# Kernel optimization log

Hardware: AMD Instinct MI355X
Metric: run time of the kernel (lower is better)

Reference implementation:

```python
import jax, jax.numpy as jnp
import numpy as np

B, N, S, K = 8, 2048, 1024, 64     # clouds, points/cloud, fps samples (ratio=0.5), max neighbors
R2 = 0.2 ** 2                      # radius^2
C_IN, H1, C_OUT = 64, 128, 256     # PointNetConv nn = MLP([67, 128, 256])


def _fps(pos):
    """Farthest point sampling on one cloud. pos: [N,3] -> [S] int32 indices (deterministic start at point 0)."""
    dist = jnp.sum((pos - pos[0]) ** 2, axis=-1)
    idxs = jnp.zeros((S,), jnp.int32)
    def body(i, carry):
        idxs, dist = carry
        nxt = jnp.argmax(dist).astype(jnp.int32)
        dist = jnp.minimum(dist, jnp.sum((pos - pos[nxt]) ** 2, axis=-1))
        return (idxs.at[i].set(nxt), dist)
    idxs, _ = jax.lax.fori_loop(1, S, body, (idxs, dist))
    return idxs


def setup_inputs() -> dict:
    key = jax.random.key(0)
    k = jax.random.split(key, 4)
    x = jax.random.normal(k[0], (B * N, C_IN), dtype=jnp.float32)
    pos = jax.random.uniform(k[1], (B * N, 3), dtype=jnp.float32)
    batch = jnp.repeat(jnp.arange(B, dtype=jnp.int32), N)
    w1 = jax.random.normal(k[2], (C_IN + 3, H1), dtype=jnp.float32) / np.sqrt(C_IN + 3).astype(np.float32)
    b1 = jnp.zeros((H1,), jnp.float32)
    w2 = jax.random.normal(k[3], (H1, C_OUT), dtype=jnp.float32) / np.sqrt(H1).astype(np.float32)
    b2 = jnp.zeros((C_OUT,), jnp.float32)
    return {"x": x, "pos": pos, "batch": batch, "w1": w1, "b1": b1, "w2": w2, "b2": b2}


def reference(x, pos, batch, w1, b1, w2, b2):
    xb = x.reshape(B, N, C_IN)
    posb = pos.reshape(B, N, 3)
    idx = jax.vmap(_fps)(posb)                                            # [B,S] fps centers
    q = jnp.take_along_axis(posb, idx[:, :, None], axis=1)                # [B,S,3] sampled positions
    # radius ball query: up to K nearest points within R of each center
    d2 = jnp.sum((q[:, :, None, :] - posb[:, None, :, :]) ** 2, axis=-1)  # [B,S,N]
    vals, nbr = jax.lax.top_k(jnp.where(d2 <= R2, -d2, -jnp.inf), K)      # [B,S,K]
    valid = jnp.isfinite(vals)                                            # padded slots -> False
    # gather edge features (PointNetConv message: nn(cat([x_j, pos_j - pos_i])))
    x_j = jax.vmap(lambda xc, nc: xc[nc])(xb, nbr)                        # [B,S,K,C_IN]
    pos_j = jax.vmap(lambda pc, nc: pc[nc])(posb, nbr)                    # [B,S,K,3]
    feat = jnp.concatenate([x_j, pos_j - q[:, :, None, :]], axis=-1)      # [B,S,K,C_IN+3]
    h = jax.nn.relu(feat @ w1 + b1) @ w2 + b2                             # [B,S,K,C_OUT]
    # masked max-aggregation over the neighborhood (empty -> 0, matching PyG scatter-max default)
    h = jnp.where(valid[..., None], h, -jnp.inf)
    out = jnp.max(h, axis=2)
    out = jnp.where(jnp.isfinite(out), out, 0.0)                          # [B,S,C_OUT]
    batch_out = jnp.repeat(jnp.arange(B, dtype=batch.dtype), S)
    return out.reshape(B * S, C_OUT), q.reshape(B * S, 3), batch_out
```

## Files before the change

kernel.cpp:

```cpp
#include <hip/hip_runtime.h>
#include <math.h>

#define BQ 8
#define NQ 2048
#define SQ 1024
#define KQ 64
#define CIN 64
#define H1Q 128
#define COUT 256
#define R2F 0.04f
#define CAP 512
#define XW_ROWS 16
#define XW_BLOCKS ((BQ*NQ)/XW_ROWS)
#define W2C_BLOCKS 16

typedef float f32x2 __attribute__((ext_vector_type(2)));
typedef float f32x4v __attribute__((ext_vector_type(4)));
typedef short bf16x8 __attribute__((ext_vector_type(8)));
typedef unsigned int u32;
typedef unsigned short u16;

__device__ __forceinline__ u16 f2bf(float f) {
    u32 u = __builtin_bit_cast(u32, f);
    return (u16)((u + 0x7FFFu + ((u >> 16) & 1u)) >> 16);
}

template <int CTRL>
__device__ __forceinline__ float maxdpp(float x) {
    int xi = __builtin_bit_cast(int, x);
    int yi = __builtin_amdgcn_update_dpp((int)0xFF800000, xi, CTRL, 0xF, 0xF, false);
    return fmaxf(x, __builtin_bit_cast(float, yi));
}

__global__ __launch_bounds__(256)
void fps_xw_kernel(const float* __restrict__ pos, int* __restrict__ idx_out,
                   float* __restrict__ q_out, float* __restrict__ batch_out,
                   const float* __restrict__ x, const float* __restrict__ w1,
                   const float* __restrict__ b1, float* __restrict__ xw,
                   const float* __restrict__ w2, u16* __restrict__ w2f) {
#pragma clang fp contract(off)
    __shared__ float lnpos[NQ][4];
    __shared__ int   sel[SQ];
    __shared__ alignas(16) u32 red[2][8];

    const int tid = threadIdx.x;

    if (blockIdx.x >= 8 + XW_BLOCKS) {
        const int cb   = (blockIdx.x - (8 + XW_BLOCKS)) * 4 + (tid >> 6);
        const int lane = tid & 63;
        const int w  = cb >> 4, ct = (cb >> 2) & 3, kt = cb & 3;
        const int n  = w*64 + ct*16 + (lane & 15);
        const int k0 = kt*32 + (lane >> 4)*8;
        u32 pk[4];
#pragma unroll
        for (int jp = 0; jp < 4; ++jp) {
            u16 lo = f2bf(w2[(size_t)(k0 + 2*jp    )*COUT + n]);
            u16 hi = f2bf(w2[(size_t)(k0 + 2*jp + 1)*COUT + n]);
            pk[jp] = (u32)lo | ((u32)hi << 16);
        }
        u32* dst = (u32*)(w2f + ((size_t)cb*64 + lane)*8);
        dst[0] = pk[0]; dst[1] = pk[1]; dst[2] = pk[2]; dst[3] = pk[3];
        return;
    }

    if (blockIdx.x >= 8) {
        __shared__ float xs[XW_ROWS][CIN];
        const int r0 = (blockIdx.x - 8) * XW_ROWS;
        for (int i = tid; i < XW_ROWS*CIN; i += 256)
            xs[i >> 6][i & 63] = x[(size_t)(r0 + (i >> 6))*CIN + (i & 63)];
        __syncthreads();
        const int h = tid & 127, rbase = (tid >> 7) * 8;
        float acc[8];
        float bb = b1[h];
#pragma unroll
        for (int r = 0; r < 8; ++r) acc[r] = bb;
        for (int c = 0; c < CIN; ++c) {
            float wv = w1[c*H1Q + h];
#pragma unroll
            for (int r = 0; r < 8; ++r)
                acc[r] = fmaf(xs[rbase + r][c], wv, acc[r]);
        }
#pragma unroll
        for (int r = 0; r < 8; ++r)
            xw[(size_t)(r0 + rbase + r)*H1Q + h] = acc[r];
        return;
    }

    const int b = blockIdx.x;
    const int lane = tid & 63, wid = tid >> 6;
    const float* p = pos + (size_t)b * NQ * 3;

    f32x2 px[4], py[4], pz[4], dist[4];
#pragma unroll
    for (int r = 0; r < 4; ++r) {
        int i0 = tid * 8 + 2 * r;
        float x0 = p[3*i0],   y0 = p[3*i0+1], z0 = p[3*i0+2];
        float x1 = p[3*i0+3], y1 = p[3*i0+4], z1 = p[3*i0+5];
        px[r] = (f32x2){x0, x1}; py[r] = (f32x2){y0, y1}; pz[r] = (f32x2){z0, z1};
        lnpos[i0][0]   = -x0; lnpos[i0][1]   = -y0; lnpos[i0][2]   = -z0; lnpos[i0][3]   = 0.f;
        lnpos[i0+1][0] = -x1; lnpos[i0+1][1] = -y1; lnpos[i0+1][2] = -z1; lnpos[i0+1][3] = 0.f;
    }
    if (tid == 0) sel[0] = 0;
    __syncthreads();

    float cx = p[0], cy = p[1], cz = p[2];
    float lmax;
    {
        f32x2 ncx = (f32x2){-cx, -cx}, ncy = (f32x2){-cy, -cy}, ncz = (f32x2){-cz, -cz};
        lmax = -INFINITY;
#pragma unroll
        for (int r = 0; r < 4; ++r) {
            f32x2 dx = px[r] + ncx, dy = py[r] + ncy, dz = pz[r] + ncz;
            f32x2 a = dx * dx, bb = dy * dy, cc = dz * dz;
            f32x2 s = (a + bb) + cc;
            dist[r] = s;
            lmax = fmaxf(fmaxf(lmax, s.x), s.y);
        }
    }

    for (int s = 1; s < SQ; ++s) {
        const int par = s & 1;

        int ra = 1000, rb = 1000;
#pragma unroll
        for (int r = 3; r >= 0; --r) {
            ra = (dist[r].x == lmax) ? 2*r     : ra;
            rb = (dist[r].y == lmax) ? 2*r + 1 : rb;
        }
        int ridx = min(ra, rb);

        float m = lmax;
        m = maxdpp<0x111>(m);
        m = maxdpp<0x112>(m);
        m = maxdpp<0x114>(m);
        m = maxdpp<0x118>(m);
        m = maxdpp<0x142>(m);
        m = maxdpp<0x143>(m);
        float wmax = __builtin_bit_cast(
            float, __builtin_amdgcn_readlane(__builtin_bit_cast(int, m), 63));

        unsigned long long msk = __ballot(lmax == wmax);
        int wl = __ffsll(msk) - 1;
        int rw = __builtin_amdgcn_readlane(ridx, wl);
        u32 widx = (u32)((wl << 3) + rw + (wid << 9));

        if (lane == 0) {
            red[par][wid*2    ] = __builtin_bit_cast(u32, wmax);
            red[par][wid*2 + 1] = widx;
        }
        __syncthreads();

        uint4 c01 = *(const uint4*)&red[par][0];
        uint4 c23 = *(const uint4*)&red[par][4];
        u32 bv = c01.x, bi = c01.y;
        if (c01.z > bv || (c01.z == bv && c01.w < bi)) { bv = c01.z; bi = c01.w; }
        if (c23.x > bv || (c23.x == bv && c23.y < bi)) { bv = c23.x; bi = c23.y; }
        if (c23.z > bv || (c23.z == bv && c23.w < bi)) { bv = c23.z; bi = c23.w; }
        if (tid == 0) sel[s] = (int)bi;

        float4 nc4 = *reinterpret_cast<const float4*>(&lnpos[bi][0]);
        f32x2 ncx = (f32x2){nc4.x, nc4.x};
        f32x2 ncy = (f32x2){nc4.y, nc4.y};
        f32x2 ncz = (f32x2){nc4.z, nc4.z};

        float nm = -INFINITY;
#pragma unroll
        for (int r = 0; r < 4; ++r) {
            f32x2 dx = px[r] + ncx, dy = py[r] + ncy, dz = pz[r] + ncz;
            f32x2 a = dx * dx, bb = dy * dy, cc = dz * dz;
            f32x2 nd = (a + bb) + cc;
            f32x2 v = __builtin_elementwise_min(dist[r], nd);
            dist[r] = v;
            nm = fmaxf(fmaxf(nm, v.x), v.y);
        }
        lmax = nm;
    }
    __syncthreads();

    for (int s = tid; s < SQ; s += 256) {
        int id = sel[s];
        idx_out[b*SQ + s] = id;
        q_out[(size_t)(b*SQ + s)*3 + 0] = -lnpos[id][0];
        q_out[(size_t)(b*SQ + s)*3 + 1] = -lnpos[id][1];
        q_out[(size_t)(b*SQ + s)*3 + 2] = -lnpos[id][2];
        batch_out[b*SQ + s] = (float)b;
    }
}

__global__ __launch_bounds__(256)
void ball_kernel(const float* __restrict__ pos, const float* __restrict__ q,
                 int* __restrict__ nbr, int* __restrict__ cnt_out) {
    const int cidx = blockIdx.x;
    const int b = cidx >> 10;
    __shared__ float sd2[CAP];
    __shared__ int   sid[CAP];
    __shared__ int   s_cnt, s_w;
    if (threadIdx.x == 0) { s_cnt = 0; s_w = 0; }
    __syncthreads();

    const float qx = q[(size_t)cidx*3], qy = q[(size_t)cidx*3+1], qz = q[(size_t)cidx*3+2];
    const float* p = pos + (size_t)b * NQ * 3;
    for (int i = threadIdx.x; i < NQ; i += 256) {
        float dx = __fsub_rn(qx, p[3*i]);
        float dy = __fsub_rn(qy, p[3*i+1]);
        float dz = __fsub_rn(qz, p[3*i+2]);
        float d2 = __fadd_rn(__fadd_rn(__fmul_rn(dx, dx), __fmul_rn(dy, dy)),
                             __fmul_rn(dz, dz));
        if (d2 <= R2F) {
            int slot = atomicAdd(&s_cnt, 1);
            if (slot < CAP) { sd2[slot] = d2; sid[slot] = i; }
        }
    }
    __syncthreads();
    int cnt = min(s_cnt, CAP);
    if (cnt <= KQ) {
        for (int t = threadIdx.x; t < cnt; t += 256) nbr[(size_t)cidx*KQ + t] = sid[t];
        if (threadIdx.x == 0) cnt_out[cidx] = cnt;
    } else {
        for (int t = threadIdx.x; t < cnt; t += 256) {
            float d = sd2[t]; int id = sid[t];
            int rank = 0;
            for (int u = 0; u < cnt; ++u) {
                float du = sd2[u];
                rank += (du < d || (du == d && sid[u] < id)) ? 1 : 0;
            }
            if (rank < KQ) { int w = atomicAdd(&s_w, 1); nbr[(size_t)cidx*KQ + w] = id; }
        }
        if (threadIdx.x == 0) cnt_out[cidx] = KQ;
    }
}

__global__ __launch_bounds__(256)
void conv_kernel(const float* __restrict__ pos, const float* __restrict__ q,
                 const int* __restrict__ nbr, const int* __restrict__ cnt_in,
                 const float* __restrict__ xw, const float* __restrict__ w1,
                 const u16* __restrict__ w2f, const float* __restrict__ b2,
                 float* __restrict__ out) {
    const int cidx = blockIdx.x;
    const int b = cidx >> 10;
    const int tid = threadIdx.x;
    __shared__ u16  hs[KQ * H1Q];
    __shared__ float dxs[KQ], dys[KQ], dzs[KQ];
    __shared__ int   js[KQ];

    const int cnt = cnt_in[cidx];
    if (cnt == 0) {
        out[(size_t)cidx*COUT + tid] = 0.0f;
        return;
    }
    const float qx = q[(size_t)cidx*3], qy = q[(size_t)cidx*3+1], qz = q[(size_t)cidx*3+2];
    const float* p = pos + (size_t)b * NQ * 3;
    if (tid < cnt) {
        int j = nbr[(size_t)cidx*KQ + tid];
        js[tid]  = j;
        dxs[tid] = p[3*j]   - qx;
        dys[tid] = p[3*j+1] - qy;
        dzs[tid] = p[3*j+2] - qz;
    }
    __syncthreads();

    const float* w1p = w1 + (size_t)CIN * H1Q;
    for (int f2 = tid; f2 < KQ*(H1Q/2); f2 += 256) {
        int e = f2 >> 6, hp = (f2 & 63) * 2;
        u32 pack;
        if (e < cnt) {
            int j = js[e];
            const f32x2 xv = *(const f32x2*)(xw + ((size_t)b*NQ + j)*H1Q + hp);
            float dx = dxs[e], dy = dys[e], dz = dzs[e];
            float v0 = xv.x, v1 = xv.y;
            v0 = fmaf(dx, w1p[hp],       v0);
            v0 = fmaf(dy, w1p[H1Q+hp],   v0);
            v0 = fmaf(dz, w1p[2*H1Q+hp], v0);
            v1 = fmaf(dx, w1p[hp+1],       v1);
            v1 = fmaf(dy, w1p[H1Q+hp+1],   v1);
            v1 = fmaf(dz, w1p[2*H1Q+hp+1], v1);
            v0 = fmaxf(v0, 0.0f); v1 = fmaxf(v1, 0.0f);
            pack = (u32)f2bf(v0) | ((u32)f2bf(v1) << 16);
        } else {
            pack = 0u;
        }
        u32 byte = (u32)e*256 + (((u32)hp*2) ^ (((u32)e & 7) << 4));
        *(u32*)((char*)hs + byte) = pack;
    }
    __syncthreads();

    const int w    = tid >> 6;
    const int lane = tid & 63;
    const int row  = lane & 15;
    const int lg   = lane >> 4;

    f32x4v acc[16];
#pragma unroll
    for (int i = 0; i < 16; ++i) acc[i] = (f32x4v){0.f, 0.f, 0.f, 0.f};

#pragma unroll
    for (int kt = 0; kt < 4; ++kt) {
        bf16x8 a[4];
#pragma unroll
        for (int mt = 0; mt < 4; ++mt) {
            u32 byte = (u32)(mt*16 + row)*256
                     + (((u32)(kt*64 + lg*16)) ^ (((u32)row & 7) << 4));
            a[mt] = *(const bf16x8*)((const char*)hs + byte);
        }
#pragma unroll
        for (int ct = 0; ct < 4; ++ct) {
            const int chunk = (w*4 + ct)*4 + kt;
            bf16x8 bf = *(const bf16x8*)(w2f + ((size_t)chunk*64 + lane)*8);
#pragma unroll
            for (int mt = 0; mt < 4; ++mt)
                acc[ct*4 + mt] = __builtin_amdgcn_mfma_f32_16x16x32_bf16(
                    a[mt], bf, acc[ct*4 + mt], 0, 0, 0);
        }
    }

#pragma unroll
    for (int ct = 0; ct < 4; ++ct) {
        float v = -INFINITY;
#pragma unroll
        for (int mt = 0; mt < 4; ++mt) {
#pragma unroll
            for (int r = 0; r < 4; ++r) {
                int rrow = mt*16 + lg*4 + r;
                float av = acc[ct*4 + mt][r];
                v = fmaxf(v, rrow < cnt ? av : -INFINITY);
            }
        }
        v = fmaxf(v, __shfl_xor(v, 16));
        v = fmaxf(v, __shfl_xor(v, 32));
        int n = w*64 + ct*16 + row;
        if (lg == 0) out[(size_t)cidx*COUT + n] = v + b2[n];
    }
}

extern "C" void kernel_launch(void* const* d_in, const int* in_sizes, int n_in,
                              void* d_out, int out_size, void* d_ws, size_t ws_size,
                              hipStream_t stream) {
    const float* x   = (const float*)d_in[0];
    const float* pos = (const float*)d_in[1];
    const float* w1  = (const float*)d_in[3];
    const float* b1  = (const float*)d_in[4];
    const float* w2  = (const float*)d_in[5];
    const float* b2  = (const float*)d_in[6];

    float* out  = (float*)d_out;
    float* qbuf = out + (size_t)BQ*SQ*COUT;
    float* bbuf = qbuf + (size_t)BQ*SQ*3;

    char* ws = (char*)d_ws;
    int*   idx = (int*)(ws);
    int*   cnt = (int*)(ws + 32768);
    int*   nbr = (int*)(ws + 65536);
    float* xw  = (float*)(ws + 65536 + (size_t)BQ*SQ*KQ*4);
    u16*   w2f = (u16*)(ws + 65536 + (size_t)BQ*SQ*KQ*4
                            + (size_t)BQ*NQ*H1Q*4);

    const int grid = 8 + XW_BLOCKS + W2C_BLOCKS;
    fps_xw_kernel<<<grid, 256, 0, stream>>>(pos, idx, qbuf, bbuf,
                                            x, w1, b1, xw, w2, w2f);
    ball_kernel  <<<BQ*SQ, 256, 0, stream>>>(pos, qbuf, nbr, cnt);
    conv_kernel  <<<BQ*SQ, 256, 0, stream>>>(pos, qbuf, nbr, cnt, xw, w1,
                                             w2f, b2, out);
}
```

Baseline: 621.9 us.

## Fuse ball query into conv kernel and broadcast FPS winner coords via reduction

Merges the ball-query and conv kernels so neighbor indices and counts stay in shared memory instead of round-tripping through a global buffer, removing one launch. In the FPS loop, each wave now carries the winning point's coordinates through the cross-wave reduction, so the next center is read from registers rather than from an LDS lookup that depends on the reduced index. The fused kernel uses more shared memory per block, which may reduce occupancy.

```diff
diff --git a/kernel.cpp b/kernel.cpp
--- a/kernel.cpp
+++ b/kernel.cpp
@@ -32,6 +32,10 @@
     return fmaxf(x, __builtin_bit_cast(float, yi));
 }
 
+__device__ __forceinline__ u32 rdlane_u(u32 v, int l) {
+    return (u32)__builtin_amdgcn_readlane((int)v, l);
+}
+
 __global__ __launch_bounds__(256)
 void fps_xw_kernel(const float* __restrict__ pos, int* __restrict__ idx_out,
                    float* __restrict__ q_out, float* __restrict__ batch_out,
@@ -41,7 +45,7 @@
 #pragma clang fp contract(off)
     __shared__ float lnpos[NQ][4];
     __shared__ int   sel[SQ];
-    __shared__ alignas(16) u32 red[2][8];
+    __shared__ alignas(16) u32 red[2][5][4];
 
     const int tid = threadIdx.x;
 
@@ -129,6 +133,20 @@
         }
         int ridx = min(ra, rb);
 
+        int pr = ridx >> 1;
+        f32x2 sx0 = (pr & 1) ? px[1] : px[0];
+        f32x2 sx1 = (pr & 1) ? px[3] : px[2];
+        f32x2 sxx = (pr & 2) ? sx1 : sx0;
+        float candx = (ridx & 1) ? sxx.y : sxx.x;
+        f32x2 sy0 = (pr & 1) ? py[1] : py[0];
+        f32x2 sy1 = (pr & 1) ? py[3] : py[2];
+        f32x2 syy = (pr & 2) ? sy1 : sy0;
+        float candy = (ridx & 1) ? syy.y : syy.x;
+        f32x2 sz0 = (pr & 1) ? pz[1] : pz[0];
+        f32x2 sz1 = (pr & 1) ? pz[3] : pz[2];
+        f32x2 szz = (pr & 2) ? sz1 : sz0;
+        float candz = (ridx & 1) ? szz.y : szz.x;
+
         float m = lmax;
         m = maxdpp<0x111>(m);
         m = maxdpp<0x112>(m);
@@ -142,26 +160,43 @@
         unsigned long long msk = __ballot(lmax == wmax);
         int wl = __ffsll(msk) - 1;
         int rw = __builtin_amdgcn_readlane(ridx, wl);
+        u32 cxb = rdlane_u(__builtin_bit_cast(u32, candx), wl);
+        u32 cyb = rdlane_u(__builtin_bit_cast(u32, candy), wl);
+        u32 czb = rdlane_u(__builtin_bit_cast(u32, candz), wl);
         u32 widx = (u32)((wl << 3) + rw + (wid << 9));
 
         if (lane == 0) {
-            red[par][wid*2    ] = __builtin_bit_cast(u32, wmax);
-            red[par][wid*2 + 1] = widx;
+            red[par][0][wid] = __builtin_bit_cast(u32, wmax);
+            red[par][1][wid] = widx;
+            red[par][2][wid] = cxb;
+            red[par][3][wid] = cyb;
+            red[par][4][wid] = czb;
         }
         __syncthreads();
 
-        uint4 c01 = *(const uint4*)&red[par][0];
-        uint4 c23 = *(const uint4*)&red[par][4];
-        u32 bv = c01.x, bi = c01.y;
-        if (c01.z > bv || (c01.z == bv && c01.w < bi)) { bv = c01.z; bi = c01.w; }
-        if (c23.x > bv || (c23.x == bv && c23.y < bi)) { bv = c23.x; bi = c23.y; }
-        if (c23.z > bv || (c23.z == bv && c23.w < bi)) { bv = c23.z; bi = c23.w; }
+        uint4 v4 = *(const uint4*)&red[par][0][0];
+        uint4 i4 = *(const uint4*)&red[par][1][0];
+        uint4 x4 = *(const uint4*)&red[par][2][0];
+        uint4 y4 = *(const uint4*)&red[par][3][0];
+        uint4 z4 = *(const uint4*)&red[par][4][0];
+
+        bool a1 = (i4.y < i4.x) ? (v4.y >= v4.x) : (v4.y > v4.x);
+        bool b1 = (i4.w < i4.z) ? (v4.w >= v4.z) : (v4.w > v4.z);
+        u32 vA = a1 ? v4.y : v4.x, iA = a1 ? i4.y : i4.x;
+        u32 vB = b1 ? v4.w : v4.z, iB = b1 ? i4.w : i4.z;
+        bool t1 = (iB < iA) ? (vB >= vA) : (vB > vA);
+        u32 bi  = t1 ? iB : iA;
+        u32 fxb = t1 ? (b1 ? x4.w : x4.z) : (a1 ? x4.y : x4.x);
+        u32 fyb = t1 ? (b1 ? y4.w : y4.z) : (a1 ? y4.y : y4.x);
+        u32 fzb = t1 ? (b1 ? z4.w : z4.z) : (a1 ? z4.y : z4.x);
         if (tid == 0) sel[s] = (int)bi;
 
-        float4 nc4 = *reinterpret_cast<const float4*>(&lnpos[bi][0]);
-        f32x2 ncx = (f32x2){nc4.x, nc4.x};
-        f32x2 ncy = (f32x2){nc4.y, nc4.y};
-        f32x2 ncz = (f32x2){nc4.z, nc4.z};
+        float ncxs = __builtin_bit_cast(float, fxb ^ 0x80000000u);
+        float ncys = __builtin_bit_cast(float, fyb ^ 0x80000000u);
+        float nczs = __builtin_bit_cast(float, fzb ^ 0x80000000u);
+        f32x2 ncx = (f32x2){ncxs, ncxs};
+        f32x2 ncy = (f32x2){ncys, ncys};
+        f32x2 ncz = (f32x2){nczs, nczs};
 
         float nm = -INFINITY;
 #pragma unroll
@@ -188,19 +223,26 @@
 }
 
 __global__ __launch_bounds__(256)
-void ball_kernel(const float* __restrict__ pos, const float* __restrict__ q,
-                 int* __restrict__ nbr, int* __restrict__ cnt_out) {
+void ballconv_kernel(const float* __restrict__ pos, const float* __restrict__ q,
+                     const float* __restrict__ xw, const float* __restrict__ w1,
+                     const u16* __restrict__ w2f, const float* __restrict__ b2,
+                     float* __restrict__ out) {
     const int cidx = blockIdx.x;
     const int b = cidx >> 10;
+    const int tid = threadIdx.x;
     __shared__ float sd2[CAP];
     __shared__ int   sid[CAP];
     __shared__ int   s_cnt, s_w;
-    if (threadIdx.x == 0) { s_cnt = 0; s_w = 0; }
+    __shared__ u16   hs[KQ * H1Q];
+    __shared__ float dxs[KQ], dys[KQ], dzs[KQ];
+    __shared__ int   js[KQ];
+
+    if (tid == 0) { s_cnt = 0; s_w = 0; }
     __syncthreads();
 
     const float qx = q[(size_t)cidx*3], qy = q[(size_t)cidx*3+1], qz = q[(size_t)cidx*3+2];
     const float* p = pos + (size_t)b * NQ * 3;
-    for (int i = threadIdx.x; i < NQ; i += 256) {
+    for (int i = tid; i < NQ; i += 256) {
         float dx = __fsub_rn(qx, p[3*i]);
         float dy = __fsub_rn(qy, p[3*i+1]);
         float dz = __fsub_rn(qz, p[3*i+2]);
@@ -213,51 +255,37 @@
     }
     __syncthreads();
     int cnt = min(s_cnt, CAP);
-    if (cnt <= KQ) {
-        for (int t = threadIdx.x; t < cnt; t += 256) nbr[(size_t)cidx*KQ + t] = sid[t];
-        if (threadIdx.x == 0) cnt_out[cidx] = cnt;
-    } else {
-        for (int t = threadIdx.x; t < cnt; t += 256) {
+
+    if (cnt > KQ) {
+        for (int t = tid; t < cnt; t += 256) {
             float d = sd2[t]; int id = sid[t];
             int rank = 0;
             for (int u = 0; u < cnt; ++u) {
                 float du = sd2[u];
                 rank += (du < d || (du == d && sid[u] < id)) ? 1 : 0;
             }
-            if (rank < KQ) { int w = atomicAdd(&s_w, 1); nbr[(size_t)cidx*KQ + w] = id; }
-        }
-        if (threadIdx.x == 0) cnt_out[cidx] = KQ;
-    }
-}
-
-__global__ __launch_bounds__(256)
-void conv_kernel(const float* __restrict__ pos, const float* __restrict__ q,
-                 const int* __restrict__ nbr, const int* __restrict__ cnt_in,
-                 const float* __restrict__ xw, const float* __restrict__ w1,
-                 const u16* __restrict__ w2f, const float* __restrict__ b2,
-                 float* __restrict__ out) {
-    const int cidx = blockIdx.x;
-    const int b = cidx >> 10;
-    const int tid = threadIdx.x;
-    __shared__ u16  hs[KQ * H1Q];
-    __shared__ float dxs[KQ], dys[KQ], dzs[KQ];
-    __shared__ int   js[KQ];
-
-    const int cnt = cnt_in[cidx];
+            if (rank < KQ) {
+                int w = atomicAdd(&s_w, 1);
+                js[w]  = id;
+                dxs[w] = p[3*id]   - qx;
+                dys[w] = p[3*id+1] - qy;
+                dzs[w] = p[3*id+2] - qz;
+            }
+        }
+        cnt = KQ;
+    } else if (tid < cnt) {
+        int id = sid[tid];
+        js[tid]  = id;
+        dxs[tid] = p[3*id]   - qx;
+        dys[tid] = p[3*id+1] - qy;
+        dzs[tid] = p[3*id+2] - qz;
+    }
+    __syncthreads();
+
     if (cnt == 0) {
         out[(size_t)cidx*COUT + tid] = 0.0f;
         return;
     }
-    const float qx = q[(size_t)cidx*3], qy = q[(size_t)cidx*3+1], qz = q[(size_t)cidx*3+2];
-    const float* p = pos + (size_t)b * NQ * 3;
-    if (tid < cnt) {
-        int j = nbr[(size_t)cidx*KQ + tid];
-        js[tid]  = j;
-        dxs[tid] = p[3*j]   - qx;
-        dys[tid] = p[3*j+1] - qy;
-        dzs[tid] = p[3*j+2] - qz;
-    }
-    __syncthreads();
 
     const float* w1p = w1 + (size_t)CIN * H1Q;
     for (int f2 = tid; f2 < KQ*(H1Q/2); f2 += 256) {
@@ -348,16 +376,11 @@
 
     char* ws = (char*)d_ws;
     int*   idx = (int*)(ws);
-    int*   cnt = (int*)(ws + 32768);
-    int*   nbr = (int*)(ws + 65536);
-    float* xw  = (float*)(ws + 65536 + (size_t)BQ*SQ*KQ*4);
-    u16*   w2f = (u16*)(ws + 65536 + (size_t)BQ*SQ*KQ*4
-                            + (size_t)BQ*NQ*H1Q*4);
+    float* xw  = (float*)(ws + 65536);
+    u16*   w2f = (u16*)(ws + 65536 + (size_t)BQ*NQ*H1Q*4);
 
     const int grid = 8 + XW_BLOCKS + W2C_BLOCKS;
-    fps_xw_kernel<<<grid, 256, 0, stream>>>(pos, idx, qbuf, bbuf,
-                                            x, w1, b1, xw, w2, w2f);
-    ball_kernel  <<<BQ*SQ, 256, 0, stream>>>(pos, qbuf, nbr, cnt);
-    conv_kernel  <<<BQ*SQ, 256, 0, stream>>>(pos, qbuf, nbr, cnt, xw, w1,
-                                             w2f, b2, out);
-}
+    fps_xw_kernel  <<<grid, 256, 0, stream>>>(pos, idx, qbuf, bbuf,
+                                              x, w1, b1, xw, w2, w2f);
+    ballconv_kernel<<<BQ*SQ, 256, 0, stream>>>(pos, qbuf, xw, w1, w2f, b2, out);
+}
```

New measurement: 741.5 us. +19.2%, slower.

## Fuse FPS, ball query and conv into one persistent producer-consumer kernel

Applied to the files above, without the earlier changes.

Merges the three kernels into a single launch. FPS blocks publish the sampled indices in chunks of 32 through global progress counters, and consumer blocks spin-wait on these so that ball query and conv for early centers overlap the serial FPS loop. Ball query and conv are also fused per center, which drops the global nbr/cnt round trip. The risks are spin-wait deadlock if the consumer blocks occupy the GPU before the producers are scheduled, polling overhead, and extra memset and fence costs. FPS blocks raise their priority to reduce contention.

```diff
diff --git a/kernel.cpp b/kernel.cpp
--- a/kernel.cpp
+++ b/kernel.cpp
@@ -13,6 +13,8 @@
 #define XW_ROWS 16
 #define XW_BLOCKS ((BQ*NQ)/XW_ROWS)
 #define W2C_BLOCKS 16
+#define CONS_BASE (8 + XW_BLOCKS + W2C_BLOCKS)
+#define READY_TARGET (XW_BLOCKS + W2C_BLOCKS)
 
 typedef float f32x2 __attribute__((ext_vector_type(2)));
 typedef float f32x4v __attribute__((ext_vector_type(4)));
@@ -33,17 +35,173 @@
 }
 
 __global__ __launch_bounds__(256)
-void fps_xw_kernel(const float* __restrict__ pos, int* __restrict__ idx_out,
-                   float* __restrict__ q_out, float* __restrict__ batch_out,
-                   const float* __restrict__ x, const float* __restrict__ w1,
-                   const float* __restrict__ b1, float* __restrict__ xw,
-                   const float* __restrict__ w2, u16* __restrict__ w2f) {
+void fused_kernel(const float* __restrict__ pos,
+                  float* __restrict__ q_out, float* __restrict__ batch_out,
+                  const float* __restrict__ x, const float* __restrict__ w1,
+                  const float* __restrict__ b1, float* __restrict__ xw,
+                  const float* __restrict__ w2, u16* __restrict__ w2f,
+                  const float* __restrict__ b2, float* __restrict__ out,
+                  int* __restrict__ selg, int* __restrict__ progress,
+                  int* __restrict__ ready) {
 #pragma clang fp contract(off)
-    __shared__ float lnpos[NQ][4];
-    __shared__ int   sel[SQ];
-    __shared__ alignas(16) u32 red[2][8];
-
+    __shared__ __align__(16) char smem[36928];
     const int tid = threadIdx.x;
+
+    if (blockIdx.x >= CONS_BASE) {
+        u16*   hs  = (u16*)smem;
+        float* sd2 = (float*)(smem + 16384);
+        int*   sid = (int*)(smem + 18432);
+        float* dxs = (float*)(smem + 20480);
+        float* dys = (float*)(smem + 20736);
+        float* dzs = (float*)(smem + 20992);
+        int*   js  = (int*)(smem + 21248);
+        int*   s_cnt = (int*)(smem + 21504);
+        int*   s_w   = (int*)(smem + 21508);
+        float* sqv   = (float*)(smem + 21512);
+
+        const int cblk = blockIdx.x - CONS_BASE;
+        const int s = cblk >> 3;
+        const int b = cblk & 7;
+        const int cidx = b*SQ + s;
+        const float* p = pos + (size_t)b * NQ * 3;
+
+        if (tid == 0) {
+            const int need = (s >> 5) + 1;
+            while (atomicAdd(&progress[b], 0) < need)
+                __builtin_amdgcn_s_sleep(127);
+            __threadfence();
+            int gidx = selg[b*SQ + s];
+            sqv[0] = p[3*gidx]; sqv[1] = p[3*gidx+1]; sqv[2] = p[3*gidx+2];
+            *s_cnt = 0; *s_w = 0;
+        }
+        __syncthreads();
+        const float qx = sqv[0], qy = sqv[1], qz = sqv[2];
+
+        for (int i = tid; i < NQ; i += 256) {
+            float dx = __fsub_rn(qx, p[3*i]);
+            float dy = __fsub_rn(qy, p[3*i+1]);
+            float dz = __fsub_rn(qz, p[3*i+2]);
+            float d2 = __fadd_rn(__fadd_rn(__fmul_rn(dx, dx), __fmul_rn(dy, dy)),
+                                 __fmul_rn(dz, dz));
+            if (d2 <= R2F) {
+                int slot = atomicAdd(s_cnt, 1);
+                if (slot < CAP) { sd2[slot] = d2; sid[slot] = i; }
+            }
+        }
+        __syncthreads();
+        int cnt = min(*s_cnt, CAP);
+
+        if (cnt > KQ) {
+            for (int t = tid; t < cnt; t += 256) {
+                float d = sd2[t]; int id = sid[t];
+                int rank = 0;
+                for (int u = 0; u < cnt; ++u) {
+                    float du = sd2[u];
+                    rank += (du < d || (du == d && sid[u] < id)) ? 1 : 0;
+                }
+                if (rank < KQ) {
+                    int w = atomicAdd(s_w, 1);
+                    js[w]  = id;
+                    dxs[w] = p[3*id]   - qx;
+                    dys[w] = p[3*id+1] - qy;
+                    dzs[w] = p[3*id+2] - qz;
+                }
+            }
+            cnt = KQ;
+        } else if (tid < cnt) {
+            int id = sid[tid];
+            js[tid]  = id;
+            dxs[tid] = p[3*id]   - qx;
+            dys[tid] = p[3*id+1] - qy;
+            dzs[tid] = p[3*id+2] - qz;
+        }
+        __syncthreads();
+
+        if (cnt == 0) {
+            out[(size_t)cidx*COUT + tid] = 0.0f;
+            return;
+        }
+
+        if (tid == 0) {
+            while (atomicAdd(ready, 0) < READY_TARGET)
+                __builtin_amdgcn_s_sleep(127);
+        }
+        __syncthreads();
+        __threadfence();
+
+        const float* w1p = w1 + (size_t)CIN * H1Q;
+        for (int f2 = tid; f2 < KQ*(H1Q/2); f2 += 256) {
+            int e = f2 >> 6, hp = (f2 & 63) * 2;
+            u32 pack;
+            if (e < cnt) {
+                int j = js[e];
+                const f32x2 xv = *(const f32x2*)(xw + ((size_t)b*NQ + j)*H1Q + hp);
+                float dx = dxs[e], dy = dys[e], dz = dzs[e];
+                float v0 = xv.x, v1 = xv.y;
+                v0 = fmaf(dx, w1p[hp],       v0);
+                v0 = fmaf(dy, w1p[H1Q+hp],   v0);
+                v0 = fmaf(dz, w1p[2*H1Q+hp], v0);
+                v1 = fmaf(dx, w1p[hp+1],       v1);
+                v1 = fmaf(dy, w1p[H1Q+hp+1],   v1);
+                v1 = fmaf(dz, w1p[2*H1Q+hp+1], v1);
+                v0 = fmaxf(v0, 0.0f); v1 = fmaxf(v1, 0.0f);
+                pack = (u32)f2bf(v0) | ((u32)f2bf(v1) << 16);
+            } else {
+                pack = 0u;
+            }
+            u32 byte = (u32)e*256 + (((u32)hp*2) ^ (((u32)e & 7) << 4));
+            *(u32*)(smem + byte) = pack;
+        }
+        __syncthreads();
+
+        const int w    = tid >> 6;
+        const int lane = tid & 63;
+        const int row  = lane & 15;
+        const int lg   = lane >> 4;
+
+        f32x4v acc[16];
+#pragma unroll
+        for (int i = 0; i < 16; ++i) acc[i] = (f32x4v){0.f, 0.f, 0.f, 0.f};
+
+#pragma unroll
+        for (int kt = 0; kt < 4; ++kt) {
+            bf16x8 a[4];
+#pragma unroll
+            for (int mt = 0; mt < 4; ++mt) {
+                u32 byte = (u32)(mt*16 + row)*256
+                         + (((u32)(kt*64 + lg*16)) ^ (((u32)row & 7) << 4));
+                a[mt] = *(const bf16x8*)(smem + byte);
+            }
+#pragma unroll
+            for (int ct = 0; ct < 4; ++ct) {
+                const int chunk = (w*4 + ct)*4 + kt;
+                bf16x8 bf = *(const bf16x8*)(w2f + ((size_t)chunk*64 + lane)*8);
+#pragma unroll
+                for (int mt = 0; mt < 4; ++mt)
+                    acc[ct*4 + mt] = __builtin_amdgcn_mfma_f32_16x16x32_bf16(
+                        a[mt], bf, acc[ct*4 + mt], 0, 0, 0);
+            }
+        }
+
+#pragma unroll
+        for (int ct = 0; ct < 4; ++ct) {
+            float v = -INFINITY;
+#pragma unroll
+            for (int mt = 0; mt < 4; ++mt) {
+#pragma unroll
+                for (int r = 0; r < 4; ++r) {
+                    int rrow = mt*16 + lg*4 + r;
+                    float av = acc[ct*4 + mt][r];
+                    v = fmaxf(v, rrow < cnt ? av : -INFINITY);
+                }
+            }
+            v = fmaxf(v, __shfl_xor(v, 16));
+            v = fmaxf(v, __shfl_xor(v, 32));
+            int n = w*64 + ct*16 + row;
+            if (lg == 0) out[(size_t)cidx*COUT + n] = v + b2[n];
+        }
+        return;
+    }
 
     if (blockIdx.x >= 8 + XW_BLOCKS) {
         const int cb   = (blockIdx.x - (8 + XW_BLOCKS)) * 4 + (tid >> 6);
@@ -60,11 +218,14 @@
         }
         u32* dst = (u32*)(w2f + ((size_t)cb*64 + lane)*8);
         dst[0] = pk[0]; dst[1] = pk[1]; dst[2] = pk[2]; dst[3] = pk[3];
+        __threadfence();
+        __syncthreads();
+        if (tid == 0) atomicAdd(ready, 1);
         return;
     }
 
     if (blockIdx.x >= 8) {
-        __shared__ float xs[XW_ROWS][CIN];
+        float (*xs)[CIN] = (float(*)[CIN])smem;
         const int r0 = (blockIdx.x - 8) * XW_ROWS;
         for (int i = tid; i < XW_ROWS*CIN; i += 256)
             xs[i >> 6][i & 63] = x[(size_t)(r0 + (i >> 6))*CIN + (i & 63)];
@@ -83,12 +244,21 @@
 #pragma unroll
         for (int r = 0; r < 8; ++r)
             xw[(size_t)(r0 + rbase + r)*H1Q + h] = acc[r];
+        __threadfence();
+        __syncthreads();
+        if (tid == 0) atomicAdd(ready, 1);
         return;
     }
+
+    __builtin_amdgcn_s_setprio(1);
+    float (*lnpos)[4] = (float(*)[4])smem;
+    int*  sel        = (int*)(smem + 32768);
+    u32 (*red)[8]    = (u32(*)[8])(smem + 36864);
 
     const int b = blockIdx.x;
     const int lane = tid & 63, wid = tid >> 6;
     const float* p = pos + (size_t)b * NQ * 3;
+    int* selg_b = selg + b*SQ;
 
     f32x2 px[4], py[4], pz[4], dist[4];
 #pragma unroll
@@ -150,6 +320,14 @@
         }
         __syncthreads();
 
+        if ((s & 31) == 0) {
+            const int base = s - 32;
+            if (tid < 32) selg_b[base + tid] = sel[base + tid];
+            __threadfence();
+            __syncthreads();
+            if (tid == 0) atomicExch(&progress[b], s >> 5);
+        }
+
         uint4 c01 = *(const uint4*)&red[par][0];
         uint4 c23 = *(const uint4*)&red[par][4];
         u32 bv = c01.x, bi = c01.y;
@@ -177,158 +355,17 @@
     }
     __syncthreads();
 
+    if (tid < 32) selg_b[992 + tid] = sel[992 + tid];
+    __threadfence();
+    __syncthreads();
+    if (tid == 0) atomicExch(&progress[b], 32);
+
     for (int s = tid; s < SQ; s += 256) {
         int id = sel[s];
-        idx_out[b*SQ + s] = id;
         q_out[(size_t)(b*SQ + s)*3 + 0] = -lnpos[id][0];
         q_out[(size_t)(b*SQ + s)*3 + 1] = -lnpos[id][1];
         q_out[(size_t)(b*SQ + s)*3 + 2] = -lnpos[id][2];
         batch_out[b*SQ + s] = (float)b;
-    }
-}
-
-__global__ __launch_bounds__(256)
-void ball_kernel(const float* __restrict__ pos, const float* __restrict__ q,
-                 int* __restrict__ nbr, int* __restrict__ cnt_out) {
-    const int cidx = blockIdx.x;
-    const int b = cidx >> 10;
-    __shared__ float sd2[CAP];
-    __shared__ int   sid[CAP];
-    __shared__ int   s_cnt, s_w;
-    if (threadIdx.x == 0) { s_cnt = 0; s_w = 0; }
-    __syncthreads();
-
-    const float qx = q[(size_t)cidx*3], qy = q[(size_t)cidx*3+1], qz = q[(size_t)cidx*3+2];
-    const float* p = pos + (size_t)b * NQ * 3;
-    for (int i = threadIdx.x; i < NQ; i += 256) {
-        float dx = __fsub_rn(qx, p[3*i]);
-        float dy = __fsub_rn(qy, p[3*i+1]);
-        float dz = __fsub_rn(qz, p[3*i+2]);
-        float d2 = __fadd_rn(__fadd_rn(__fmul_rn(dx, dx), __fmul_rn(dy, dy)),
-                             __fmul_rn(dz, dz));
-        if (d2 <= R2F) {
-            int slot = atomicAdd(&s_cnt, 1);
-            if (slot < CAP) { sd2[slot] = d2; sid[slot] = i; }
-        }
-    }
-    __syncthreads();
-    int cnt = min(s_cnt, CAP);
-    if (cnt <= KQ) {
-        for (int t = threadIdx.x; t < cnt; t += 256) nbr[(size_t)cidx*KQ + t] = sid[t];
-        if (threadIdx.x == 0) cnt_out[cidx] = cnt;
-    } else {
-        for (int t = threadIdx.x; t < cnt; t += 256) {
-            float d = sd2[t]; int id = sid[t];
-            int rank = 0;
-            for (int u = 0; u < cnt; ++u) {
-                float du = sd2[u];
-                rank += (du < d || (du == d && sid[u] < id)) ? 1 : 0;
-            }
-            if (rank < KQ) { int w = atomicAdd(&s_w, 1); nbr[(size_t)cidx*KQ + w] = id; }
-        }
-        if (threadIdx.x == 0) cnt_out[cidx] = KQ;
-    }
-}
-
-__global__ __launch_bounds__(256)
-void conv_kernel(const float* __restrict__ pos, const float* __restrict__ q,
-                 const int* __restrict__ nbr, const int* __restrict__ cnt_in,
-                 const float* __restrict__ xw, const float* __restrict__ w1,
-                 const u16* __restrict__ w2f, const float* __restrict__ b2,
-                 float* __restrict__ out) {
-    const int cidx = blockIdx.x;
-    const int b = cidx >> 10;
-    const int tid = threadIdx.x;
-    __shared__ u16  hs[KQ * H1Q];
-    __shared__ float dxs[KQ], dys[KQ], dzs[KQ];
-    __shared__ int   js[KQ];
-
-    const int cnt = cnt_in[cidx];
-    if (cnt == 0) {
-        out[(size_t)cidx*COUT + tid] = 0.0f;
-        return;
-    }
-    const float qx = q[(size_t)cidx*3], qy = q[(size_t)cidx*3+1], qz = q[(size_t)cidx*3+2];
-    const float* p = pos + (size_t)b * NQ * 3;
-    if (tid < cnt) {
-        int j = nbr[(size_t)cidx*KQ + tid];
-        js[tid]  = j;
-        dxs[tid] = p[3*j]   - qx;
-        dys[tid] = p[3*j+1] - qy;
-        dzs[tid] = p[3*j+2] - qz;
-    }
-    __syncthreads();
-
-    const float* w1p = w1 + (size_t)CIN * H1Q;
-    for (int f2 = tid; f2 < KQ*(H1Q/2); f2 += 256) {
-        int e = f2 >> 6, hp = (f2 & 63) * 2;
-        u32 pack;
-        if (e < cnt) {
-            int j = js[e];
-            const f32x2 xv = *(const f32x2*)(xw + ((size_t)b*NQ + j)*H1Q + hp);
-            float dx = dxs[e], dy = dys[e], dz = dzs[e];
-            float v0 = xv.x, v1 = xv.y;
-            v0 = fmaf(dx, w1p[hp],       v0);
-            v0 = fmaf(dy, w1p[H1Q+hp],   v0);
-            v0 = fmaf(dz, w1p[2*H1Q+hp], v0);
-            v1 = fmaf(dx, w1p[hp+1],       v1);
-            v1 = fmaf(dy, w1p[H1Q+hp+1],   v1);
-            v1 = fmaf(dz, w1p[2*H1Q+hp+1], v1);
-            v0 = fmaxf(v0, 0.0f); v1 = fmaxf(v1, 0.0f);
-            pack = (u32)f2bf(v0) | ((u32)f2bf(v1) << 16);
-        } else {
-            pack = 0u;
-        }
-        u32 byte = (u32)e*256 + (((u32)hp*2) ^ (((u32)e & 7) << 4));
-        *(u32*)((char*)hs + byte) = pack;
-    }
-    __syncthreads();
-
-    const int w    = tid >> 6;
-    const int lane = tid & 63;
-    const int row  = lane & 15;
-    const int lg   = lane >> 4;
-
-    f32x4v acc[16];
-#pragma unroll
-    for (int i = 0; i < 16; ++i) acc[i] = (f32x4v){0.f, 0.f, 0.f, 0.f};
-
-#pragma unroll
-    for (int kt = 0; kt < 4; ++kt) {
-        bf16x8 a[4];
-#pragma unroll
-        for (int mt = 0; mt < 4; ++mt) {
-            u32 byte = (u32)(mt*16 + row)*256
-                     + (((u32)(kt*64 + lg*16)) ^ (((u32)row & 7) << 4));
-            a[mt] = *(const bf16x8*)((const char*)hs + byte);
-        }
-#pragma unroll
-        for (int ct = 0; ct < 4; ++ct) {
-            const int chunk = (w*4 + ct)*4 + kt;
-            bf16x8 bf = *(const bf16x8*)(w2f + ((size_t)chunk*64 + lane)*8);
-#pragma unroll
-            for (int mt = 0; mt < 4; ++mt)
-                acc[ct*4 + mt] = __builtin_amdgcn_mfma_f32_16x16x32_bf16(
-                    a[mt], bf, acc[ct*4 + mt], 0, 0, 0);
-        }
-    }
-
-#pragma unroll
-    for (int ct = 0; ct < 4; ++ct) {
-        float v = -INFINITY;
-#pragma unroll
-        for (int mt = 0; mt < 4; ++mt) {
-#pragma unroll
-            for (int r = 0; r < 4; ++r) {
-                int rrow = mt*16 + lg*4 + r;
-                float av = acc[ct*4 + mt][r];
-                v = fmaxf(v, rrow < cnt ? av : -INFINITY);
-            }
-        }
-        v = fmaxf(v, __shfl_xor(v, 16));
-        v = fmaxf(v, __shfl_xor(v, 32));
-        int n = w*64 + ct*16 + row;
-        if (lg == 0) out[(size_t)cidx*COUT + n] = v + b2[n];
     }
 }
 
@@ -347,17 +384,16 @@
     float* bbuf = qbuf + (size_t)BQ*SQ*3;
 
     char* ws = (char*)d_ws;
-    int*   idx = (int*)(ws);
-    int*   cnt = (int*)(ws + 32768);
-    int*   nbr = (int*)(ws + 65536);
-    float* xw  = (float*)(ws + 65536 + (size_t)BQ*SQ*KQ*4);
-    u16*   w2f = (u16*)(ws + 65536 + (size_t)BQ*SQ*KQ*4
-                            + (size_t)BQ*NQ*H1Q*4);
-
-    const int grid = 8 + XW_BLOCKS + W2C_BLOCKS;
-    fps_xw_kernel<<<grid, 256, 0, stream>>>(pos, idx, qbuf, bbuf,
-                                            x, w1, b1, xw, w2, w2f);
-    ball_kernel  <<<BQ*SQ, 256, 0, stream>>>(pos, qbuf, nbr, cnt);
-    conv_kernel  <<<BQ*SQ, 256, 0, stream>>>(pos, qbuf, nbr, cnt, xw, w1,
-                                             w2f, b2, out);
+    float* xw  = (float*)(ws + 65536);
+    u16*   w2f = (u16*)(ws + 65536 + (size_t)BQ*NQ*H1Q*4);
+    int*   selg = (int*)(ws + 65536 + (size_t)BQ*NQ*H1Q*4 + 65536);
+    int*   progress = selg + BQ*SQ;
+    int*   ready    = progress + BQ;
+
+    hipMemsetAsync(progress, 0, (BQ + 1) * sizeof(int), stream);
+
+    const int grid = CONS_BASE + BQ*SQ;
+    fused_kernel<<<grid, 256, 0, stream>>>(pos, qbuf, bbuf,
+                                           x, w1, b1, xw, w2, w2f,
+                                           b2, out, selg, progress, ready);
 }
```

After: 932.4 us. 49.9% more time.
